# Kernel tuning notes

Hardware: AMD Instinct MI355X
Metric: run time of the kernel (lower is better)

Reference implementation:

```python
import jax, jax.numpy as jnp
import numpy as np

N, H, M, B = 512, 64, 1024, 256
ETA = 1.0
INIT_STD = 0.01

def setup_inputs() -> dict:
    key = jax.random.key(0)
    k1, k2, k3, k4 = jax.random.split(key, 4)
    # Binary +/-1 sequences and memory (as produced upstream in the repo)
    sequences = jnp.where(jax.random.uniform(k1, (B, N)) < 0.5, -1.0, 1.0).astype(jnp.float32)
    memory = jnp.where(jax.random.uniform(k2, (M, N)) < 0.5, -1.0, 1.0).astype(jnp.float32)
    A_logits = (INIT_STD * jax.random.normal(k3, (N, H, N))).astype(jnp.float32)
    B_logits = (INIT_STD * jax.random.normal(k4, (H, N))).astype(jnp.float32)
    return {"sequences": sequences, "memory": memory, "A_logits": A_logits, "B_logits": B_logits}

def reference(sequences, memory, A_logits, B_logits):
    # Vectorized version of DAM.train_batch's loss over positions n=1..N-1.
    n_dim = sequences.shape[1]
    # Causal mask: row for position n attends to indices i < n. Rows n=1..N-1.
    ns = jnp.arange(1, n_dim)[:, None, None]            # (N-1,1,1)
    idx = jnp.arange(n_dim)[None, None, :]              # (1,1,N)
    mask = idx < ns                                      # (N-1,1,N)
    neg_inf = jnp.asarray(-jnp.inf, A_logits.dtype)
    A = jax.nn.softmax(jnp.where(mask, A_logits[1:], neg_inf), axis=-1)  # (N-1,H,N), zeros outside mask
    Bn = jax.nn.softmax(B_logits, axis=-1)               # (H,N)
    phi_mu = jnp.einsum('hn,mn->mh', Bn, memory)         # (M,H) memory keys
    hat_phi = jnp.einsum('bi,nhi->bnh', sequences, A)    # (B,N-1,H) queries for every position at once
    score = ETA * jnp.einsum('bnh,mh->bnm', hat_phi, phi_mu)  # (B,N-1,M)
    pi = jax.nn.softmax(score, axis=-1)                  # retrieval distribution over memories
    plus = (memory[:, 1:] > 0).astype(pi.dtype)          # (M,N-1): memory bit at position n is +1
    prob = jnp.einsum('bnm,mn->bn', pi, plus)            # P(next bit = +1)
    prob = jnp.clip(prob, 1e-6, 1.0 - 1e-6)
    target = (sequences[:, 1:] > 0).astype(prob.dtype)
    bce = -(target * jnp.log(prob) + (1.0 - target) * jnp.log1p(-prob))
    # mean over batch per position, summed over positions, / (N-1) == global mean
    return jnp.mean(bce)
```

## Files before the change

kernel.cpp:

```cpp
#include <hip/hip_runtime.h>
#include <stdint.h>

#define NPOS 512
#define NH   64
#define NM   1024
#define NB   256
#define NM1  511

typedef __attribute__((ext_vector_type(8)))  short bf16x8;
typedef __attribute__((ext_vector_type(16))) float f32x16;
typedef __attribute__((ext_vector_type(4)))  float f32x4;
typedef __attribute__((ext_vector_type(4)))  int   i32x4;

#if __has_builtin(__builtin_amdgcn_exp2f)
#define EXP2F(x) __builtin_amdgcn_exp2f(x)
#else
#define EXP2F(x) __expf((x) * 0.69314718055994531f)
#endif

__device__ __forceinline__ unsigned short f2bf(float x) {
    unsigned u = __float_as_uint(x);
    u = (u + 0x7FFFu + ((u >> 16) & 1u)) >> 16;
    return (unsigned short)u;
}
__device__ __forceinline__ int pack2(unsigned short a, unsigned short b) {
    return (int)a | ((int)b << 16);
}

__global__ __launch_bounds__(256, 4)
void kA_prep(const float* __restrict__ seq, const float* __restrict__ Bl,
             const float* __restrict__ mem,
             unsigned short* __restrict__ seq_bf, float* __restrict__ BnT,
             float* __restrict__ plusT, float* __restrict__ out) {
    const int bid = blockIdx.x, t = threadIdx.x;
    if (bid < 128) {
        if (bid == 0 && t == 0) out[0] = 0.f;
        int idx = (bid * 256 + t) * 4;
        f32x4 v = *(const f32x4*)(seq + idx);
        int2 o;
        o.x = pack2(f2bf(v.x), f2bf(v.y));
        o.y = pack2(f2bf(v.z), f2bf(v.w));
        *(int2*)(seq_bf + idx) = o;
    } else if (bid < 144) {
        const int h = (bid - 128) * 4 + (t >> 6), l = t & 63;
        float v[8]; float mx = -1e30f;
#pragma unroll
        for (int j = 0; j < 8; j++) { v[j] = Bl[h * NPOS + l + 64 * j]; mx = fmaxf(mx, v[j]); }
#pragma unroll
        for (int o = 32; o; o >>= 1) mx = fmaxf(mx, __shfl_xor(mx, o));
        float s = 0.f;
#pragma unroll
        for (int j = 0; j < 8; j++) { v[j] = __expf(v[j] - mx); s += v[j]; }
#pragma unroll
        for (int o = 32; o; o >>= 1) s += __shfl_xor(s, o);
        float r = 1.0f / s;
#pragma unroll
        for (int j = 0; j < 8; j++) BnT[(l + 64 * j) * NH + h] = v[j] * r;
    } else {
        __shared__ float sT[64][65];
        const int bb = bid - 144;
        const int mt = bb >> 3, nt = bb & 7;
        const int rr = t >> 2, cc = t & 3;
        const float* src = mem + (size_t)(mt * 64 + rr) * NPOS + nt * 64 + cc * 16;
#pragma unroll
        for (int j = 0; j < 4; j++) {
            f32x4 v = *(const f32x4*)(src + j * 4);
            sT[rr][cc * 16 + j * 4 + 0] = (v.x > 0.f) ? 1.f : 0.f;
            sT[rr][cc * 16 + j * 4 + 1] = (v.y > 0.f) ? 1.f : 0.f;
            sT[rr][cc * 16 + j * 4 + 2] = (v.z > 0.f) ? 1.f : 0.f;
            sT[rr][cc * 16 + j * 4 + 3] = (v.w > 0.f) ? 1.f : 0.f;
        }
        __syncthreads();
        float* dst = plusT + (size_t)(nt * 64 + rr) * NM + mt * 64 + cc * 16;
#pragma unroll
        for (int j = 0; j < 4; j++) {
            f32x4 o;
            o.x = sT[cc * 16 + j * 4 + 0][rr];
            o.y = sT[cc * 16 + j * 4 + 1][rr];
            o.z = sT[cc * 16 + j * 4 + 2][rr];
            o.w = sT[cc * 16 + j * 4 + 3][rr];
            *(f32x4*)(dst + j * 4) = o;
        }
    }
}

__global__ __launch_bounds__(256, 4)
void k1b_phimu(const float* __restrict__ BnT, const float* __restrict__ mem,
               unsigned short* __restrict__ phimu) {
    const int m0 = blockIdx.x * 2, t = threadIdx.x;
    __shared__ float mrow[2][NPOS];
    __shared__ float part[2][256];
    {
        int row = t >> 7, c = (t & 127) * 4;
        *(f32x4*)(&mrow[row][c]) = *(const f32x4*)(mem + (size_t)(m0 + row) * NPOS + c);
    }
    __syncthreads();
    const int h = t & 63, seg = t >> 6;
    float a[2] = {0.f, 0.f};
    float b2[2] = {0.f, 0.f};
    const float* bp = BnT + seg * 128 * NH + h;
#pragma unroll 8
    for (int nn = 0; nn < 128; nn += 2) {
        float x0 = bp[nn * NH], x1 = bp[(nn + 1) * NH];
#pragma unroll
        for (int row = 0; row < 2; row++) {
            a[row]  = fmaf(x0, mrow[row][seg * 128 + nn], a[row]);
            b2[row] = fmaf(x1, mrow[row][seg * 128 + nn + 1], b2[row]);
        }
    }
#pragma unroll
    for (int row = 0; row < 2; row++) part[row][t] = a[row] + b2[row];
    __syncthreads();
    if (t < 64) {
#pragma unroll
        for (int row = 0; row < 2; row++) {
            float s = (part[row][t] + part[row][t + 64]) + (part[row][t + 128] + part[row][t + 192]);
            phimu[(m0 + row) * NH + t] = f2bf(s * 1.4426950408889634f);
        }
    }
}

__global__ __launch_bounds__(256, 2)
void k23_fused(const float* __restrict__ Al, const unsigned short* __restrict__ seq_bf,
               const unsigned short* __restrict__ phimu, const float* __restrict__ plusT,
               const float* __restrict__ seq, float* __restrict__ out) {
    __shared__ __align__(16) unsigned short big[256 * 72];
    __shared__ float s_plus[NM];
    __shared__ float z_lds[64];

    const int t = threadIdx.x;
    const int n = NM1 - (int)blockIdx.x;
    const int ksteps = (n + 63) >> 6;
    const int wv = t >> 6, lane = t & 63, half = lane >> 5, r = lane & 31;

    if (t < 64) z_lds[t] = 0.f;
    *(f32x4*)(s_plus + t * 4) = *(const f32x4*)(plusT + n * NM + t * 4);

    const int eh = t >> 2, ei = (t & 3) * 16;
    const float* arow = Al + ((size_t)n * NH + eh) * NPOS + ei;
    const unsigned short* s0 = seq_bf + (size_t)(wv * 64 + r) * NPOS + half * 8;
    const unsigned short* s1 = s0 + 32 * NPOS;

    f32x16 acc00, acc01, acc10, acc11;
#pragma unroll
    for (int i = 0; i < 16; i++) { acc00[i] = 0.f; acc01[i] = 0.f; acc10[i] = 0.f; acc11[i] = 0.f; }

    f32x4 ea[4];
#pragma unroll
    for (int g = 0; g < 4; g++) ea[g] = *(const f32x4*)(arow + g * 4);

    for (int kk = 0; kk < ksteps; kk++) {
        const int k0 = kk * 64;
        unsigned short* ebuf = big + (kk & 1) * (64 * 72);
        {
            float zp = 0.f;
            int ev[8];
#pragma unroll
            for (int g = 0; g < 4; g++) {
                int i0 = k0 + ei + g * 4;
                float e0 = (i0 + 0 < n) ? __expf(ea[g].x) : 0.f;
                float e1 = (i0 + 1 < n) ? __expf(ea[g].y) : 0.f;
                float e2 = (i0 + 2 < n) ? __expf(ea[g].z) : 0.f;
                float e3 = (i0 + 3 < n) ? __expf(ea[g].w) : 0.f;
                zp += (e0 + e1) + (e2 + e3);
                ev[g * 2]     = pack2(f2bf(e0), f2bf(e1));
                ev[g * 2 + 1] = pack2(f2bf(e2), f2bf(e3));
            }
            unsigned short* ep = ebuf + eh * 72 + ei;
            *(i32x4*)(ep)     = *(i32x4*)(ev);
            *(i32x4*)(ep + 8) = *(i32x4*)(ev + 4);
            zp += __shfl_xor(zp, 1);
            zp += __shfl_xor(zp, 2);
            if ((t & 3) == 0) z_lds[eh] += zp;
        }
        if (kk + 1 < ksteps) {
#pragma unroll
            for (int g = 0; g < 4; g++) ea[g] = *(const f32x4*)(arow + k0 + 64 + g * 4);
        }
        __syncthreads();
        {
            const unsigned short* sB0 = ebuf + r * 72;
            const unsigned short* sB1 = sB0 + 32 * 72;
#pragma unroll
            for (int kq = 0; kq < 4; kq++) {
                const int ko = kq * 16;
                bf16x8 A0 = *(const bf16x8*)(s0 + k0 + ko);
                bf16x8 A1 = *(const bf16x8*)(s1 + k0 + ko);
                bf16x8 B0 = *(const bf16x8*)(sB0 + ko + half * 8);
                bf16x8 B1 = *(const bf16x8*)(sB1 + ko + half * 8);
                acc00 = __builtin_amdgcn_mfma_f32_32x32x16_bf16(A0, B0, acc00, 0, 0, 0);
                acc01 = __builtin_amdgcn_mfma_f32_32x32x16_bf16(A0, B1, acc01, 0, 0, 0);
                acc10 = __builtin_amdgcn_mfma_f32_32x32x16_bf16(A1, B0, acc10, 0, 0, 0);
                acc11 = __builtin_amdgcn_mfma_f32_32x32x16_bf16(A1, B1, acc11, 0, 0, 0);
            }
        }
    }
    __syncthreads();
    {
        float rz0 = 1.0f / z_lds[r];
        float rz1 = 1.0f / z_lds[32 + r];
#pragma unroll
        for (int reg = 0; reg < 16; reg++) {
            int row = (reg & 3) + 8 * (reg >> 2) + 4 * half;
            big[(wv * 64 + row) * 72 + r]            = f2bf(acc00[reg] * rz0);
            big[(wv * 64 + row) * 72 + 32 + r]       = f2bf(acc01[reg] * rz1);
            big[(wv * 64 + 32 + row) * 72 + r]       = f2bf(acc10[reg] * rz0);
            big[(wv * 64 + 32 + row) * 72 + 32 + r]  = f2bf(acc11[reg] * rz1);
        }
    }
    __syncthreads();

    bf16x8 p[4];
#pragma unroll
    for (int kq = 0; kq < 4; kq++)
        p[kq] = *(const bf16x8*)(phimu + (r) * NH + kq * 16 + half * 8);
    bf16x8 q[2][4];
#pragma unroll
    for (int bs = 0; bs < 2; bs++)
#pragma unroll
        for (int kq = 0; kq < 4; kq++)
            q[bs][kq] = *(const bf16x8*)(big + (wv * 64 + bs * 32 + r) * 72 + kq * 16 + half * 8);

    f32x4 den0 = {0.f,0.f,0.f,0.f}, num0 = {0.f,0.f,0.f,0.f};
    f32x4 den1 = {0.f,0.f,0.f,0.f}, num1 = {0.f,0.f,0.f,0.f};

    for (int it = 0; it < 32; ++it) {
        bf16x8 pn[4];
        if (it < 31) {
#pragma unroll
            for (int kq = 0; kq < 4; kq++)
                pn[kq] = *(const bf16x8*)(phimu + ((it + 1) * 32 + r) * NH + kq * 16 + half * 8);
        }
        f32x16 a0, a1;
#pragma unroll
        for (int i = 0; i < 16; i++) { a0[i] = 0.f; a1[i] = 0.f; }
#pragma unroll
        for (int kq = 0; kq < 4; kq++) {
            a0 = __builtin_amdgcn_mfma_f32_32x32x16_bf16(p[kq], q[0][kq], a0, 0, 0, 0);
            a1 = __builtin_amdgcn_mfma_f32_32x32x16_bf16(p[kq], q[1][kq], a1, 0, 0, 0);
        }
        const int mb = it * 32;
        f32x4 pv[4];
#pragma unroll
        for (int g = 0; g < 4; g++) pv[g] = *(const f32x4*)(s_plus + mb + 4 * half + 8 * g);
#pragma unroll
        for (int g = 0; g < 4; g++) {
            f32x4 e0, e1;
#pragma unroll
            for (int j = 0; j < 4; j++) {
                e0[j] = EXP2F(a0[4 * g + j]);
                e1[j] = EXP2F(a1[4 * g + j]);
            }
            den0 += e0; num0 += e0 * pv[g];
            den1 += e1; num1 += e1 * pv[g];
        }
        if (it < 31) {
#pragma unroll
            for (int kq = 0; kq < 4; kq++) p[kq] = pn[kq];
        }
    }
    float d0 = (den0[0] + den0[1]) + (den0[2] + den0[3]);
    float nu0 = (num0[0] + num0[1]) + (num0[2] + num0[3]);
    float d1 = (den1[0] + den1[1]) + (den1[2] + den1[3]);
    float nu1 = (num1[0] + num1[1]) + (num1[2] + num1[3]);
    d0 += __shfl_xor(d0, 32); nu0 += __shfl_xor(nu0, 32);
    d1 += __shfl_xor(d1, 32); nu1 += __shfl_xor(nu1, 32);

    float bce = 0.f;
    if (half == 0) {
        float pa = nu0 / d0;
        pa = fminf(fmaxf(pa, 1e-6f), 1.0f - 1e-6f);
        float ta = seq[(size_t)(wv * 64 + r) * NPOS + n];
        bce += (ta > 0.f) ? -logf(pa) : -logf(1.0f - pa);
        float pb = nu1 / d1;
        pb = fminf(fmaxf(pb, 1e-6f), 1.0f - 1e-6f);
        float tb = seq[(size_t)(wv * 64 + 32 + r) * NPOS + n];
        bce += (tb > 0.f) ? -logf(pb) : -logf(1.0f - pb);
    }
#pragma unroll
    for (int o = 32; o; o >>= 1) bce += __shfl_xor(bce, o);
    if (lane == 0) z_lds[wv] = bce;
    __syncthreads();
    if (t == 0)
        atomicAdd(out, (z_lds[0] + z_lds[1] + z_lds[2] + z_lds[3]) * (1.0f / 130816.0f));
}

extern "C" void kernel_launch(void* const* d_in, const int* in_sizes, int n_in,
                              void* d_out, int out_size, void* d_ws, size_t ws_size,
                              hipStream_t stream) {
    const float* seq = (const float*)d_in[0];
    const float* mem = (const float*)d_in[1];
    const float* Al  = (const float*)d_in[2];
    const float* Bl  = (const float*)d_in[3];

    char* ws = (char*)d_ws;
    unsigned short* seq_bf = (unsigned short*)(ws + 0);
    float*          BnT    = (float*)(ws + 262144);
    unsigned short* phimu  = (unsigned short*)(ws + 393216);
    float*          plusT  = (float*)(ws + 524288);
    float*          outp   = (float*)d_out;

    kA_prep<<<272, 256, 0, stream>>>(seq, Bl, mem, seq_bf, BnT, plusT, outp);
    k1b_phimu<<<512, 256, 0, stream>>>(BnT, mem, phimu);
    k23_fused<<<511, 256, 0, stream>>>(Al, seq_bf, phimu, plusT, seq, outp);
}
```

Before: 147.1 us.

## Split fused kernel work across eight waves with 512-thread blocks

Doubles the block size of the fused softmax/GEMM/retrieval kernel from 256 to 512 threads, so each wave handles 32 batch rows instead of 64. Each wave now holds two MFMA accumulators instead of four, and each thread computes exponentials for 8 logits instead of 16. This cuts per-thread register pressure and work, which should raise parallelism per block and hide latency better. The cost is more waves per block competing for one CU's resources, extra shuffle reduction steps, and an added barrier before the main loop.

After: 173.5 us. 1.18x slower.

```diff
diff --git a/kernel.cpp b/kernel.cpp
--- a/kernel.cpp
+++ b/kernel.cpp
@@ -120,7 +120,7 @@
     }
 }
 
-__global__ __launch_bounds__(256, 2)
+__global__ __launch_bounds__(512, 4)
 void k23_fused(const float* __restrict__ Al, const unsigned short* __restrict__ seq_bf,
                const unsigned short* __restrict__ phimu, const float* __restrict__ plusT,
                const float* __restrict__ seq, float* __restrict__ out) {
@@ -134,29 +134,29 @@
     const int wv = t >> 6, lane = t & 63, half = lane >> 5, r = lane & 31;
 
     if (t < 64) z_lds[t] = 0.f;
-    *(f32x4*)(s_plus + t * 4) = *(const f32x4*)(plusT + n * NM + t * 4);
-
-    const int eh = t >> 2, ei = (t & 3) * 16;
+    if (t < 256) *(f32x4*)(s_plus + t * 4) = *(const f32x4*)(plusT + n * NM + t * 4);
+
+    const int eh = t >> 3, ei = (t & 7) * 8;
     const float* arow = Al + ((size_t)n * NH + eh) * NPOS + ei;
-    const unsigned short* s0 = seq_bf + (size_t)(wv * 64 + r) * NPOS + half * 8;
-    const unsigned short* s1 = s0 + 32 * NPOS;
-
-    f32x16 acc00, acc01, acc10, acc11;
-#pragma unroll
-    for (int i = 0; i < 16; i++) { acc00[i] = 0.f; acc01[i] = 0.f; acc10[i] = 0.f; acc11[i] = 0.f; }
-
-    f32x4 ea[4];
-#pragma unroll
-    for (int g = 0; g < 4; g++) ea[g] = *(const f32x4*)(arow + g * 4);
+    const unsigned short* s0 = seq_bf + (size_t)(wv * 32 + r) * NPOS + half * 8;
+
+    f32x16 acc0, acc1;
+#pragma unroll
+    for (int i = 0; i < 16; i++) { acc0[i] = 0.f; acc1[i] = 0.f; }
+
+    f32x4 ea[2];
+    ea[0] = *(const f32x4*)(arow);
+    ea[1] = *(const f32x4*)(arow + 4);
+    __syncthreads();
 
     for (int kk = 0; kk < ksteps; kk++) {
         const int k0 = kk * 64;
         unsigned short* ebuf = big + (kk & 1) * (64 * 72);
         {
             float zp = 0.f;
-            int ev[8];
-#pragma unroll
-            for (int g = 0; g < 4; g++) {
+            int ev[4];
+#pragma unroll
+            for (int g = 0; g < 2; g++) {
                 int i0 = k0 + ei + g * 4;
                 float e0 = (i0 + 0 < n) ? __expf(ea[g].x) : 0.f;
                 float e1 = (i0 + 1 < n) ? __expf(ea[g].y) : 0.f;
@@ -166,32 +166,27 @@
                 ev[g * 2]     = pack2(f2bf(e0), f2bf(e1));
                 ev[g * 2 + 1] = pack2(f2bf(e2), f2bf(e3));
             }
-            unsigned short* ep = ebuf + eh * 72 + ei;
-            *(i32x4*)(ep)     = *(i32x4*)(ev);
-            *(i32x4*)(ep + 8) = *(i32x4*)(ev + 4);
+            *(i32x4*)(ebuf + eh * 72 + ei) = *(i32x4*)(ev);
             zp += __shfl_xor(zp, 1);
             zp += __shfl_xor(zp, 2);
-            if ((t & 3) == 0) z_lds[eh] += zp;
+            zp += __shfl_xor(zp, 4);
+            if ((t & 7) == 0) z_lds[eh] += zp;
         }
         if (kk + 1 < ksteps) {
-#pragma unroll
-            for (int g = 0; g < 4; g++) ea[g] = *(const f32x4*)(arow + k0 + 64 + g * 4);
+            ea[0] = *(const f32x4*)(arow + k0 + 64);
+            ea[1] = *(const f32x4*)(arow + k0 + 68);
         }
         __syncthreads();
         {
-            const unsigned short* sB0 = ebuf + r * 72;
+            const unsigned short* sB0 = ebuf + r * 72 + half * 8;
             const unsigned short* sB1 = sB0 + 32 * 72;
 #pragma unroll
             for (int kq = 0; kq < 4; kq++) {
-                const int ko = kq * 16;
-                bf16x8 A0 = *(const bf16x8*)(s0 + k0 + ko);
-                bf16x8 A1 = *(const bf16x8*)(s1 + k0 + ko);
-                bf16x8 B0 = *(const bf16x8*)(sB0 + ko + half * 8);
-                bf16x8 B1 = *(const bf16x8*)(sB1 + ko + half * 8);
-                acc00 = __builtin_amdgcn_mfma_f32_32x32x16_bf16(A0, B0, acc00, 0, 0, 0);
-                acc01 = __builtin_amdgcn_mfma_f32_32x32x16_bf16(A0, B1, acc01, 0, 0, 0);
-                acc10 = __builtin_amdgcn_mfma_f32_32x32x16_bf16(A1, B0, acc10, 0, 0, 0);
-                acc11 = __builtin_amdgcn_mfma_f32_32x32x16_bf16(A1, B1, acc11, 0, 0, 0);
+                bf16x8 A  = *(const bf16x8*)(s0 + k0 + kq * 16);
+                bf16x8 B0 = *(const bf16x8*)(sB0 + kq * 16);
+                bf16x8 B1 = *(const bf16x8*)(sB1 + kq * 16);
+                acc0 = __builtin_amdgcn_mfma_f32_32x32x16_bf16(A, B0, acc0, 0, 0, 0);
+                acc1 = __builtin_amdgcn_mfma_f32_32x32x16_bf16(A, B1, acc1, 0, 0, 0);
             }
         }
     }
@@ -202,10 +197,8 @@
 #pragma unroll
         for (int reg = 0; reg < 16; reg++) {
             int row = (reg & 3) + 8 * (reg >> 2) + 4 * half;
-            big[(wv * 64 + row) * 72 + r]            = f2bf(acc00[reg] * rz0);
-            big[(wv * 64 + row) * 72 + 32 + r]       = f2bf(acc01[reg] * rz1);
-            big[(wv * 64 + 32 + row) * 72 + r]       = f2bf(acc10[reg] * rz0);
-            big[(wv * 64 + 32 + row) * 72 + 32 + r]  = f2bf(acc11[reg] * rz1);
+            big[(wv * 32 + row) * 72 + r]      = f2bf(acc0[reg] * rz0);
+            big[(wv * 32 + row) * 72 + 32 + r] = f2bf(acc1[reg] * rz1);
         }
     }
     __syncthreads();
@@ -214,15 +207,12 @@
 #pragma unroll
     for (int kq = 0; kq < 4; kq++)
         p[kq] = *(const bf16x8*)(phimu + (r) * NH + kq * 16 + half * 8);
-    bf16x8 q[2][4];
-#pragma unroll
-    for (int bs = 0; bs < 2; bs++)
-#pragma unroll
-        for (int kq = 0; kq < 4; kq++)
-            q[bs][kq] = *(const bf16x8*)(big + (wv * 64 + bs * 32 + r) * 72 + kq * 16 + half * 8);
-
-    f32x4 den0 = {0.f,0.f,0.f,0.f}, num0 = {0.f,0.f,0.f,0.f};
-    f32x4 den1 = {0.f,0.f,0.f,0.f}, num1 = {0.f,0.f,0.f,0.f};
+    bf16x8 q[4];
+#pragma unroll
+    for (int kq = 0; kq < 4; kq++)
+        q[kq] = *(const bf16x8*)(big + (wv * 32 + r) * 72 + kq * 16 + half * 8);
+
+    f32x4 den = {0.f,0.f,0.f,0.f}, num = {0.f,0.f,0.f,0.f};
 
     for (int it = 0; it < 32; ++it) {
         bf16x8 pn[4];
@@ -231,58 +221,48 @@
             for (int kq = 0; kq < 4; kq++)
                 pn[kq] = *(const bf16x8*)(phimu + ((it + 1) * 32 + r) * NH + kq * 16 + half * 8);
         }
-        f32x16 a0, a1;
-#pragma unroll
-        for (int i = 0; i < 16; i++) { a0[i] = 0.f; a1[i] = 0.f; }
-#pragma unroll
-        for (int kq = 0; kq < 4; kq++) {
-            a0 = __builtin_amdgcn_mfma_f32_32x32x16_bf16(p[kq], q[0][kq], a0, 0, 0, 0);
-            a1 = __builtin_amdgcn_mfma_f32_32x32x16_bf16(p[kq], q[1][kq], a1, 0, 0, 0);
-        }
+        f32x16 a;
+#pragma unroll
+        for (int i = 0; i < 16; i++) a[i] = 0.f;
+#pragma unroll
+        for (int kq = 0; kq < 4; kq++)
+            a = __builtin_amdgcn_mfma_f32_32x32x16_bf16(p[kq], q[kq], a, 0, 0, 0);
         const int mb = it * 32;
-        f32x4 pv[4];
-#pragma unroll
-        for (int g = 0; g < 4; g++) pv[g] = *(const f32x4*)(s_plus + mb + 4 * half + 8 * g);
 #pragma unroll
         for (int g = 0; g < 4; g++) {
-            f32x4 e0, e1;
-#pragma unroll
-            for (int j = 0; j < 4; j++) {
-                e0[j] = EXP2F(a0[4 * g + j]);
-                e1[j] = EXP2F(a1[4 * g + j]);
-            }
-            den0 += e0; num0 += e0 * pv[g];
-            den1 += e1; num1 += e1 * pv[g];
+            f32x4 pv = *(const f32x4*)(s_plus + mb + 4 * half + 8 * g);
+            f32x4 e;
+#pragma unroll
+            for (int j = 0; j < 4; j++)
+                e[j] = EXP2F(a[4 * g + j]);
+            den += e; num += e * pv;
         }
         if (it < 31) {
 #pragma unroll
             for (int kq = 0; kq < 4; kq++) p[kq] = pn[kq];
         }
     }
-    float d0 = (den0[0] + den0[1]) + (den0[2] + den0[3]);
-    float nu0 = (num0[0] + num0[1]) + (num0[2] + num0[3]);
-    float d1 = (den1[0] + den1[1]) + (den1[2] + den1[3]);
-    float nu1 = (num1[0] + num1[1]) + (num1[2] + num1[3]);
-    d0 += __shfl_xor(d0, 32); nu0 += __shfl_xor(nu0, 32);
-    d1 += __shfl_xor(d1, 32); nu1 += __shfl_xor(nu1, 32);
+    float d  = (den[0] + den[1]) + (den[2] + den[3]);
+    float nu = (num[0] + num[1]) + (num[2] + num[3]);
+    d += __shfl_xor(d, 32); nu += __shfl_xor(nu, 32);
 
     float bce = 0.f;
     if (half == 0) {
-        float pa = nu0 / d0;
-        pa = fminf(fmaxf(pa, 1e-6f), 1.0f - 1e-6f);
-        float ta = seq[(size_t)(wv * 64 + r) * NPOS + n];
-        bce += (ta > 0.f) ? -logf(pa) : -logf(1.0f - pa);
-        float pb = nu1 / d1;
-        pb = fminf(fmaxf(pb, 1e-6f), 1.0f - 1e-6f);
-        float tb = seq[(size_t)(wv * 64 + 32 + r) * NPOS + n];
-        bce += (tb > 0.f) ? -logf(pb) : -logf(1.0f - pb);
+        float p2 = nu / d;
+        p2 = fminf(fmaxf(p2, 1e-6f), 1.0f - 1e-6f);
+        float tg = seq[(size_t)(wv * 32 + r) * NPOS + n];
+        bce = (tg > 0.f) ? -logf(p2) : -logf(1.0f - p2);
     }
 #pragma unroll
     for (int o = 32; o; o >>= 1) bce += __shfl_xor(bce, o);
     if (lane == 0) z_lds[wv] = bce;
     __syncthreads();
-    if (t == 0)
-        atomicAdd(out, (z_lds[0] + z_lds[1] + z_lds[2] + z_lds[3]) * (1.0f / 130816.0f));
+    if (t == 0) {
+        float s = 0.f;
+#pragma unroll
+        for (int w = 0; w < 8; w++) s += z_lds[w];
+        atomicAdd(out, s * (1.0f / 130816.0f));
+    }
 }
 
 extern "C" void kernel_launch(void* const* d_in, const int* in_sizes, int n_in,
@@ -302,5 +282,5 @@
 
     kA_prep<<<272, 256, 0, stream>>>(seq, Bl, mem, seq_bf, BnT, plusT, outp);
     k1b_phimu<<<512, 256, 0, stream>>>(BnT, mem, phimu);
-    k23_fused<<<511, 256, 0, stream>>>(Al, seq_bf, phimu, plusT, seq, outp);
-}
+    k23_fused<<<511, 512, 0, stream>>>(Al, seq_bf, phimu, plusT, seq, outp);
+}
```
